# Performance work log

Hardware: AMD Instinct MI355X
Metric: run time of the kernel (lower is better)

Reference implementation:

```python
import jax, jax.numpy as jnp
import numpy as np

NC = 151  # number of object classes (VG)
NR = 51   # number of relation classes (VG)


def setup_inputs() -> dict:
    key = jax.random.key(0)
    ks = jax.random.split(key, 10)
    B, N, D = 32, 100, 4096
    H = D // 4
    w = lambda k, shape, fan_in: (jax.random.normal(k, shape, jnp.float32) / np.sqrt(fan_in).astype(np.float32))
    return {
        "encoder_reps": jax.random.normal(ks[0], (B * N, D), jnp.float32),
        "W_comp": w(ks[1], (D, H), D),        # obj_comp Linear (no bias)
        "W_ou1": w(ks[2], (H, H), H),         # ou1 Linear
        "W_ofc": w(ks[3], (H, H), H),         # ofc_u Linear
        "W_decomp": w(ks[4], (H, D), H),      # obj_decomp Linear
        "conv1": w(ks[5], (10, NR, 3, 3), NR * 9),  # Conv2d(51,10,3,pad=1)
        "conv2": w(ks[6], (5, 10, 3, 3), 10 * 9),   # Conv2d(10,5,3,pad=1)
        "conv3": w(ks[7], (1, 5, 1, 1), 5),         # Conv2d(5,1,1)
        "freq_emb": jax.random.normal(ks[8], (NC * NC, NR), jnp.float32) * 0.01,
        "obj_preds": jax.random.randint(ks[9], (B * N,), 0, NC),
        "num_obj": 100,
    }


def reference(encoder_reps, W_comp, W_ou1, W_ofc, W_decomp, conv1, conv2, conv3, freq_emb, obj_preds, num_obj):
    T, D = encoder_reps.shape
    N = num_obj
    B = T // N
    relu = jax.nn.relu
    # obj_comp then per-image ou1 (vectorized over images)
    comp = relu(encoder_reps @ W_comp).reshape(B, N, -1)   # [B,N,H]
    obj_u1 = relu(comp @ W_ou1)                             # [B,N,H]
    # product-index frequency-bias gather: emb[subj*NC + obj]
    labels = obj_preds.reshape(B, N)
    pair_idx = labels[:, :, None] * NC + labels[:, None, :]  # [B,N,N]
    adj_fg = freq_emb[pair_idx]                               # [B,N,N,NR]
    # adjacency net: Conv-Conv-Conv-Tanh over the NxN 'image' with NR channels
    x = jnp.transpose(adj_fg, (0, 3, 1, 2))                   # [B,NR,N,N]
    dn = ("NCHW", "OIHW", "NCHW")
    x = jax.lax.conv_general_dilated(x, conv1, (1, 1), "SAME", dimension_numbers=dn)
    x = jax.lax.conv_general_dilated(x, conv2, (1, 1), "SAME", dimension_numbers=dn)
    x = jnp.tanh(jax.lax.conv_general_dilated(x, conv3, (1, 1), "SAME", dimension_numbers=dn))
    adj = x[:, 0]                                             # [B,N,N]
    # graph message passing: adj @ obj_u1, then ofc_u / decomp + residual
    ofl_u = jnp.einsum("bnm,bmh->bnh", adj, obj_u1).reshape(T, -1)
    u_m = relu(ofl_u @ W_ofc)
    decomp = relu(u_m @ W_decomp)
    return decomp + encoder_reps
```

## Files before the change

### kernel.cpp

```cpp
#include <hip/hip_runtime.h>
#include <cmath>

#define NCC 151
#define NRCH 51
#define BDIM 32
#define NOBJ 100
#define DDIM 4096
#define HDIM 1024
#define TDIM (BDIM * NOBJ)

typedef __bf16 bf16_t;
typedef __bf16 bf16x8 __attribute__((ext_vector_type(8)));
typedef __bf16 bf16x4 __attribute__((ext_vector_type(4)));
typedef float f32x4 __attribute__((ext_vector_type(4)));

template <bool RELU, bool ADDBF16, int SPLITK, int MODE>
__global__ __launch_bounds__(256) void gemm_bf16(
    const bf16_t* __restrict__ A,
    const bf16_t* __restrict__ Bt,
    const bf16_t* __restrict__ add,
    void* __restrict__ Cout,
    int N, int K, size_t MN) {
  __shared__ __align__(16) bf16_t Asm[128 * 64];
  __shared__ __align__(16) bf16_t Bsm[128 * 64];
  const int tid = threadIdx.x;
  const int lane = tid & 63;
  const int w = tid >> 6;
  const int wm = w >> 1, wn = w & 1;

  const int nx = gridDim.x, ny = gridDim.y, nz = gridDim.z;
  const int h = blockIdx.x + nx * (blockIdx.y + ny * blockIdx.z);
  int bx, by, bz;
  if (MODE == 3) {
    const int xcd = h & 7, s = h >> 3;
    bz = xcd >> 1;
    const int half = xcd & 1;
    if (half == 1 && s >= 96) return;
    const int c = s / 40;
    if (c < 2) {
      const int within = s % 40;
      bx = within / 5;
      by = (half ? 13 : 0) + c * 5 + within % 5;
    } else if (half == 0) {
      const int w2 = s - 80;
      bx = w2 / 3;
      by = 10 + w2 % 3;
    } else {
      const int w2 = s - 80;
      bx = w2 / 2;
      by = 23 + w2 % 2;
    }
  } else {
    const int nwg = nx * ny * nz;
    const int q = nwg >> 3;
    const int lin = (h & 7) * q + (h >> 3);
    by = lin % ny;
    const int r = lin / ny;
    bx = r % nx;
    bz = r / nx;
  }

  const int bm = by * 128, bn = bx * 128;
  const int lr = lane & 15, lk = lane >> 4;

  int kBeg = 0, kEnd = K;
  if (SPLITK > 1) {
    const int chunk = (((K / 64) + SPLITK - 1) / SPLITK) * 64;
    kBeg = bz * chunk;
    kEnd = min(K, kBeg + chunk);
  }

  f32x4 acc[4][4];
#pragma unroll
  for (int m = 0; m < 4; ++m)
#pragma unroll
    for (int n = 0; n < 4; ++n) acc[m][n] = (f32x4){0.f, 0.f, 0.f, 0.f};

  const int srow = tid >> 3, sslot = tid & 7;
  char* ldsA = (char*)Asm;
  char* ldsB = (char*)Bsm;

  for (int kt = kBeg; kt < kEnd; kt += 64) {
    __syncthreads();
#pragma unroll
    for (int i = 0; i < 4; ++i) {
      const int row = i * 32 + srow;
      const int kc = sslot ^ (row & 7);
      const bf16_t* ga = A + (size_t)(bm + row) * K + kt + kc * 8;
      const bf16_t* gb = Bt + (size_t)(bn + row) * K + kt + kc * 8;
      __builtin_amdgcn_global_load_lds(
          (const __attribute__((address_space(1))) void*)ga,
          (__attribute__((address_space(3))) void*)(ldsA + i * 4096 + w * 1024),
          16, 0, 0);
      __builtin_amdgcn_global_load_lds(
          (const __attribute__((address_space(1))) void*)gb,
          (__attribute__((address_space(3))) void*)(ldsB + i * 4096 + w * 1024),
          16, 0, 0);
    }
    __syncthreads();

    bf16x8 af[4][2], bfr[4][2];
#pragma unroll
    for (int m = 0; m < 4; ++m) {
      const int row = wm * 64 + m * 16 + lr;
#pragma unroll
      for (int kk = 0; kk < 2; ++kk) {
        const int slot = kk * 4 + lk;
        af[m][kk] =
            *(const bf16x8*)(ldsA + row * 128 + ((slot ^ (lr & 7)) << 4));
      }
    }
#pragma unroll
    for (int n = 0; n < 4; ++n) {
      const int row = wn * 64 + n * 16 + lr;
#pragma unroll
      for (int kk = 0; kk < 2; ++kk) {
        const int slot = kk * 4 + lk;
        bfr[n][kk] =
            *(const bf16x8*)(ldsB + row * 128 + ((slot ^ (lr & 7)) << 4));
      }
    }
#pragma unroll
    for (int m = 0; m < 4; ++m)
#pragma unroll
      for (int n = 0; n < 4; ++n) {
        acc[m][n] = __builtin_amdgcn_mfma_f32_16x16x32_bf16(
            af[m][0], bfr[n][0], acc[m][n], 0, 0, 0);
        acc[m][n] = __builtin_amdgcn_mfma_f32_16x16x32_bf16(
            af[m][1], bfr[n][1], acc[m][n], 0, 0, 0);
      }
  }

  const int or0 = bm + wm * 64 + lk * 4;
  const int oc0 = bn + wn * 64 + lr;
#pragma unroll
  for (int m = 0; m < 4; ++m)
#pragma unroll
    for (int n = 0; n < 4; ++n)
#pragma unroll
      for (int r = 0; r < 4; ++r) {
        float v = acc[m][n][r];
        const size_t off = (size_t)(or0 + m * 16 + r) * N + (oc0 + n * 16);
        if (SPLITK > 1) {
          ((bf16_t*)Cout)[bz * MN + off] = (bf16_t)v;
        } else {
          if (RELU) v = fmaxf(v, 0.f);
          if (ADDBF16)
            ((float*)Cout)[off] = v + (float)add[off];
          else
            ((bf16_t*)Cout)[off] = (bf16_t)v;
        }
      }
}

template <int NPART>
__global__ __launch_bounds__(256) void reduceN_kernel(
    const bf16_t* __restrict__ p, bf16_t* __restrict__ out, int n8,
    size_t MN) {
  int i = blockIdx.x * 256 + threadIdx.x;
  if (i >= n8) return;
  float s[8] = {};
#pragma unroll
  for (int z = 0; z < NPART; ++z) {
    bf16x8 v = *(const bf16x8*)(p + z * MN + (size_t)i * 8);
#pragma unroll
    for (int j = 0; j < 8; ++j) s[j] += (float)v[j];
  }
  bf16x8 o;
#pragma unroll
  for (int j = 0; j < 8; ++j) o[j] = (bf16_t)fmaxf(s[j], 0.f);
  *(bf16x8*)(out + (size_t)i * 8) = o;
}

__global__ __launch_bounds__(256) void prep_all(
    const float* __restrict__ enc, const float* __restrict__ Wcomp,
    const float* __restrict__ Wou1, const float* __restrict__ Wofc,
    const float* __restrict__ Wdec, const float* __restrict__ w1,
    bf16_t* __restrict__ encb, bf16_t* __restrict__ WcompT,
    bf16_t* __restrict__ Wou1T, bf16_t* __restrict__ WofcT,
    bf16_t* __restrict__ WdecT, float* __restrict__ w1r) {
  __shared__ float t[32][33];
  const int tid = threadIdx.x;
  int blk = blockIdx.x;

  if (blk < 12800) {
    const int i = blk * 256 + tid;
    float4 v = ((const float4*)enc)[i];
    bf16x4 o = {(bf16_t)v.x, (bf16_t)v.y, (bf16_t)v.z, (bf16_t)v.w};
    ((bf16x4*)encb)[i] = o;
    return;
  }
  blk -= 12800;

  const float* in;
  bf16_t* out;
  int K, N, nx;
  if (blk < 4096) {
    in = Wcomp; out = WcompT; K = 4096; N = 1024; nx = 32;
  } else if (blk < 4096 + 1024) {
    blk -= 4096;
    in = Wou1; out = Wou1T; K = 1024; N = 1024; nx = 32;
  } else if (blk < 4096 + 2048) {
    blk -= 4096 + 1024;
    in = Wofc; out = WofcT; K = 1024; N = 1024; nx = 32;
  } else if (blk < 4096 + 2048 + 4096) {
    blk -= 4096 + 2048;
    in = Wdec; out = WdecT; K = 1024; N = 4096; nx = 128;
  } else {
    blk -= 4096 + 2048 + 4096;
    const int idx = blk * 256 + tid;
    if (idx < NRCH * 90) {
      int ci = idx / 90, r = idx % 90, k9 = r / 10, co = r % 10;
      w1r[idx] = w1[((co * NRCH + ci) * 3 + k9 / 3) * 3 + (k9 % 3)];
    }
    return;
  }

  const int n0 = (blk % nx) * 32, k0 = (blk / nx) * 32;
  const int tx = tid & 31, ty = tid >> 5;
#pragma unroll
  for (int i = 0; i < 4; ++i)
    t[ty + i * 8][tx] = in[(size_t)(k0 + ty + i * 8) * N + n0 + tx];
  __syncthreads();
#pragma unroll
  for (int i = 0; i < 4; ++i)
    out[(size_t)(n0 + ty + i * 8) * K + k0 + tx] = (bf16_t)t[tx][ty + i * 8];
}

__global__ __launch_bounds__(128) void femb1_kernel(
    const float* __restrict__ femb, const float* __restrict__ w1r,
    float* __restrict__ femb1) {
  __shared__ float row[NRCH];
  const int p = blockIdx.x;
  if (threadIdx.x < NRCH)
    row[threadIdx.x] = femb[(size_t)p * NRCH + threadIdx.x];
  __syncthreads();
  const int t = threadIdx.x;
  if (t >= 90) return;
  float acc = 0.f;
#pragma unroll
  for (int ci = 0; ci < NRCH; ++ci) acc += row[ci] * w1r[ci * 90 + t];
  femb1[((size_t)p * 9 + t / 10) * 12 + (t % 10)] = acc;
}

__global__ __launch_bounds__(256) void conv_fused(
    const int* __restrict__ preds, const float* __restrict__ femb1,
    const float* __restrict__ w2, const float* __restrict__ w3,
    float* __restrict__ adj) {
  __shared__ float xt[18][18][12];
  __shared__ float w[90];
  const int tid = threadIdx.x;
  const int b = blockIdx.z;
  const int ti = blockIdx.y * 16, tj = blockIdx.x * 16;

  if (tid < 90) {
    const int k9 = tid / 10, c2 = tid % 10;
    float a = 0.f;
#pragma unroll
    for (int c3 = 0; c3 < 5; ++c3)
      a += w3[c3] * w2[(c3 * 10 + c2) * 9 + k9];
    w[tid] = a;
  }

  const int* pr = preds + b * NOBJ;

  for (int t = tid; t < 324; t += 256) {
    const int hi = t / 18, wj = t % 18;
    const int ii = ti - 1 + hi, jj = tj - 1 + wj;
    f32x4 a0 = {0.f, 0.f, 0.f, 0.f}, a1 = a0, a2 = a0;
    if (ii >= 0 && ii < NOBJ && jj >= 0 && jj < NOBJ) {
#pragma unroll
      for (int kh = 0; kh < 3; ++kh) {
        const int i2 = ii + kh - 1;
        if (i2 < 0 || i2 >= NOBJ) continue;
        const int li = pr[i2];
#pragma unroll
        for (int kw = 0; kw < 3; ++kw) {
          const int j2 = jj + kw - 1;
          if (j2 < 0 || j2 >= NOBJ) continue;
          const int p = li * NCC + pr[j2];
          const f32x4* f =
              (const f32x4*)(femb1 + ((size_t)p * 9 + kh * 3 + kw) * 12);
          a0 += f[0];
          a1 += f[1];
          a2 += f[2];
        }
      }
    }
    f32x4* o = (f32x4*)&xt[hi][wj][0];
    o[0] = a0;
    o[1] = a1;
    o[2] = a2;
  }
  __syncthreads();

  const int di = tid >> 4, dj = tid & 15;
  const int i = ti + di, j = tj + dj;
  if (i >= NOBJ || j >= NOBJ) return;
  float acc = 0.f;
#pragma unroll
  for (int kh = 0; kh < 3; ++kh)
#pragma unroll
    for (int kw = 0; kw < 3; ++kw) {
      const float* xr = &xt[di + kh][dj + kw][0];
      const float* wr = w + (kh * 3 + kw) * 10;
#pragma unroll
      for (int c = 0; c < 10; ++c) acc += wr[c] * xr[c];
    }
  adj[((size_t)b * NOBJ + i) * NOBJ + j] = tanhf(acc);
}

__global__ __launch_bounds__(256) void einsum_mfma_kernel(
    const float* __restrict__ adj, const bf16_t* __restrict__ u1,
    bf16_t* __restrict__ ofl) {
  __shared__ __align__(16) bf16_t As[128 * 128];
  __shared__ __align__(16) bf16_t Us[128 * 128];
  const int b = blockIdx.y;
  const int h0 = blockIdx.x * 128;
  const int tid = threadIdx.x, lane = tid & 63, w = tid >> 6;
  const int wm = w >> 1, wn = w & 1;
  const int lr = lane & 15, lk = lane >> 4;

  {
    f32x4 z = {0.f, 0.f, 0.f, 0.f};
#pragma unroll
    for (int i = 0; i < 8; ++i) ((f32x4*)As)[tid + i * 256] = z;
#pragma unroll
    for (int i = 0; i < 8; ++i) ((f32x4*)Us)[tid + i * 256] = z;
  }
  __syncthreads();

  const float* ab = adj + (size_t)b * 10000;
#pragma unroll
  for (int i = 0; i < 10; ++i) {
    int idx = tid + i * 256;
    if (idx < 2500) {
      int row = idx / 25, kc = idx % 25;
      f32x4 v = ((const f32x4*)ab)[idx];
      bf16x4 o = {(bf16_t)v[0], (bf16_t)v[1], (bf16_t)v[2], (bf16_t)v[3]};
      int slot = kc >> 1;
      *(bf16x4*)((char*)As + row * 256 + ((slot ^ (row & 7)) << 4) +
                 (kc & 1) * 8) = o;
    }
  }

  const bf16_t* ub = u1 + (size_t)b * 100 * HDIM + h0;
#pragma unroll
  for (int i = 0; i < 7; ++i) {
    int idx = tid + i * 256;
    if (idx < 1600) {
      int hc = idx / 100, m = idx % 100;
      bf16x8 v = *(const bf16x8*)(ub + (size_t)m * HDIM + hc * 8);
      int slot = m >> 3, mr = m & 7;
#pragma unroll
      for (int j = 0; j < 8; ++j) {
        int h = hc * 8 + j;
        *((bf16_t*)((char*)Us + h * 256 + ((slot ^ (h & 7)) << 4) + mr * 2)) =
            v[j];
      }
    }
  }
  __syncthreads();

  f32x4 acc[4][4];
#pragma unroll
  for (int m = 0; m < 4; ++m)
#pragma unroll
    for (int n = 0; n < 4; ++n) acc[m][n] = (f32x4){0.f, 0.f, 0.f, 0.f};

#pragma unroll
  for (int ks = 0; ks < 4; ++ks) {
    bf16x8 a[4], u[4];
#pragma unroll
    for (int m = 0; m < 4; ++m) {
      int row = wm * 64 + m * 16 + lr;
      int slot = ks * 4 + lk;
      a[m] = *(const bf16x8*)((char*)As + row * 256 + ((slot ^ (lr & 7)) << 4));
    }
#pragma unroll
    for (int n = 0; n < 4; ++n) {
      int row = wn * 64 + n * 16 + lr;
      int slot = ks * 4 + lk;
      u[n] = *(const bf16x8*)((char*)Us + row * 256 + ((slot ^ (lr & 7)) << 4));
    }
#pragma unroll
    for (int m = 0; m < 4; ++m)
#pragma unroll
      for (int n = 0; n < 4; ++n)
        acc[m][n] = __builtin_amdgcn_mfma_f32_16x16x32_bf16(a[m], u[n],
                                                            acc[m][n], 0, 0, 0);
  }

  const int or0 = wm * 64 + lk * 4;
  const int oc0 = h0 + wn * 64 + lr;
#pragma unroll
  for (int m = 0; m < 4; ++m)
#pragma unroll
    for (int n = 0; n < 4; ++n)
#pragma unroll
      for (int r = 0; r < 4; ++r) {
        int row = or0 + m * 16 + r;
        if (row < 100)
          ofl[((size_t)b * 100 + row) * HDIM + oc0 + n * 16] =
              (bf16_t)acc[m][n][r];
      }
}

extern "C" void kernel_launch(void* const* d_in, const int* in_sizes, int n_in,
                              void* d_out, int out_size, void* d_ws,
                              size_t ws_size, hipStream_t stream) {
  const float* enc = (const float*)d_in[0];
  const float* W_comp = (const float*)d_in[1];
  const float* W_ou1 = (const float*)d_in[2];
  const float* W_ofc = (const float*)d_in[3];
  const float* W_dec = (const float*)d_in[4];
  const float* conv1w = (const float*)d_in[5];
  const float* conv2w = (const float*)d_in[6];
  const float* conv3w = (const float*)d_in[7];
  const float* femb = (const float*)d_in[8];
  const int* preds = (const int*)d_in[9];
  float* out = (float*)d_out;
  char* wsb = (char*)d_ws;

  const size_t MN = (size_t)TDIM * HDIM;

  bf16_t* encb   = (bf16_t*)(wsb + 0);
  bf16_t* WcompT = (bf16_t*)(wsb + 26214400);
  bf16_t* Wou1T  = (bf16_t*)(wsb + 34603008);
  bf16_t* WofcT  = (bf16_t*)(wsb + 36700160);
  bf16_t* WdecT  = (bf16_t*)(wsb + 38797312);
  float*  w1r    = (float*)(wsb + 47185920);
  bf16_t* comp   = (bf16_t*)(wsb + 47204352);
  bf16_t* part4  = (bf16_t*)(wsb + 53757952);
  float*  femb1  = (float*)(wsb + 53757952);
  bf16_t* obj_u1 = (bf16_t*)(wsb + 63608064);
  float*  adj    = (float*)(wsb + 70161664);
  bf16_t* u_m    = (bf16_t*)(wsb + 71441664);
  bf16_t* ofl_u  = (bf16_t*)(wsb + 47204352);

  const int n8 = (int)(MN / 8);

  prep_all<<<23058, 256, 0, stream>>>(enc, W_comp, W_ou1, W_ofc, W_dec,
                                      conv1w, encb, WcompT, Wou1T, WofcT,
                                      WdecT, w1r);

  gemm_bf16<false, false, 4, 3><<<dim3(832, 1, 1), 256, 0, stream>>>(
      encb, WcompT, nullptr, part4, HDIM, DDIM, MN);
  reduceN_kernel<4><<<n8 / 256, 256, 0, stream>>>(part4, comp, n8, MN);

  gemm_bf16<true, false, 1, 0>
      <<<dim3(HDIM / 128, TDIM / 128), 256, 0, stream>>>(
          comp, Wou1T, nullptr, obj_u1, HDIM, HDIM, MN);

  femb1_kernel<<<NCC * NCC, 128, 0, stream>>>(femb, w1r, femb1);
  conv_fused<<<dim3(7, 7, BDIM), 256, 0, stream>>>(preds, femb1, conv2w,
                                                   conv3w, adj);

  einsum_mfma_kernel<<<dim3(HDIM / 128, BDIM), 256, 0, stream>>>(adj, obj_u1,
                                                                 ofl_u);

  gemm_bf16<true, false, 1, 0>
      <<<dim3(HDIM / 128, TDIM / 128), 256, 0, stream>>>(
          ofl_u, WofcT, nullptr, u_m, HDIM, HDIM, MN);

  gemm_bf16<true, true, 1, 0>
      <<<dim3(DDIM / 128, TDIM / 128), 256, 0, stream>>>(
          u_m, WdecT, encb, out, DDIM, HDIM, MN);
}
```

Baseline: 243.2 us.

## Co-schedule conv1 precompute with split-K GEMM and reduce with conv

```diff
diff --git a/kernel.cpp b/kernel.cpp
--- a/kernel.cpp
+++ b/kernel.cpp
@@ -8,6 +8,7 @@
 #define DDIM 4096
 #define HDIM 1024
 #define TDIM (BDIM * NOBJ)
+#define NPAIR (NCC * NCC)
 
 typedef __bf16 bf16_t;
 typedef __bf16 bf16x8 __attribute__((ext_vector_type(8)));
@@ -16,10 +17,8 @@
 
 template <bool RELU, bool ADDBF16, int SPLITK, int MODE>
 __global__ __launch_bounds__(256) void gemm_bf16(
-    const bf16_t* __restrict__ A,
-    const bf16_t* __restrict__ Bt,
-    const bf16_t* __restrict__ add,
-    void* __restrict__ Cout,
+    const bf16_t* __restrict__ A, const bf16_t* __restrict__ Bt,
+    const bf16_t* __restrict__ add, void* __restrict__ Cout,
     int N, int K, size_t MN) {
   __shared__ __align__(16) bf16_t Asm[128 * 64];
   __shared__ __align__(16) bf16_t Bsm[128 * 64];
@@ -31,26 +30,7 @@
   const int nx = gridDim.x, ny = gridDim.y, nz = gridDim.z;
   const int h = blockIdx.x + nx * (blockIdx.y + ny * blockIdx.z);
   int bx, by, bz;
-  if (MODE == 3) {
-    const int xcd = h & 7, s = h >> 3;
-    bz = xcd >> 1;
-    const int half = xcd & 1;
-    if (half == 1 && s >= 96) return;
-    const int c = s / 40;
-    if (c < 2) {
-      const int within = s % 40;
-      bx = within / 5;
-      by = (half ? 13 : 0) + c * 5 + within % 5;
-    } else if (half == 0) {
-      const int w2 = s - 80;
-      bx = w2 / 3;
-      by = 10 + w2 % 3;
-    } else {
-      const int w2 = s - 80;
-      bx = w2 / 2;
-      by = 23 + w2 % 2;
-    }
-  } else {
+  {
     const int nwg = nx * ny * nz;
     const int q = nwg >> 3;
     const int lin = (h & 7) * q + (h >> 3);
@@ -153,112 +133,180 @@
       }
 }
 
-template <int NPART>
-__global__ __launch_bounds__(256) void reduceN_kernel(
-    const bf16_t* __restrict__ p, bf16_t* __restrict__ out, int n8,
+__global__ __launch_bounds__(256) void fused_g1_femb1(
+    const bf16_t* __restrict__ A,
+    const bf16_t* __restrict__ Bt,
+    bf16_t* __restrict__ part4,
+    const float* __restrict__ femb,
+    const float* __restrict__ w1,
+    float* __restrict__ femb1,
     size_t MN) {
-  int i = blockIdx.x * 256 + threadIdx.x;
-  if (i >= n8) return;
-  float s[8] = {};
-#pragma unroll
-  for (int z = 0; z < NPART; ++z) {
-    bf16x8 v = *(const bf16x8*)(p + z * MN + (size_t)i * 8);
-#pragma unroll
-    for (int j = 0; j < 8; ++j) s[j] += (float)v[j];
-  }
-  bf16x8 o;
-#pragma unroll
-  for (int j = 0; j < 8; ++j) o[j] = (bf16_t)fmaxf(s[j], 0.f);
-  *(bf16x8*)(out + (size_t)i * 8) = o;
-}
-
-__global__ __launch_bounds__(256) void prep_all(
-    const float* __restrict__ enc, const float* __restrict__ Wcomp,
-    const float* __restrict__ Wou1, const float* __restrict__ Wofc,
-    const float* __restrict__ Wdec, const float* __restrict__ w1,
-    bf16_t* __restrict__ encb, bf16_t* __restrict__ WcompT,
-    bf16_t* __restrict__ Wou1T, bf16_t* __restrict__ WofcT,
-    bf16_t* __restrict__ WdecT, float* __restrict__ w1r) {
-  __shared__ float t[32][33];
   const int tid = threadIdx.x;
   int blk = blockIdx.x;
 
-  if (blk < 12800) {
-    const int i = blk * 256 + tid;
-    float4 v = ((const float4*)enc)[i];
-    bf16x4 o = {(bf16_t)v.x, (bf16_t)v.y, (bf16_t)v.z, (bf16_t)v.w};
-    ((bf16x4*)encb)[i] = o;
+  if (blk >= 832) {
+    __shared__ float w1s[10 * NRCH * 9];
+    __shared__ float rows[2][NRCH];
+    for (int t = tid; t < 10 * NRCH * 9; t += 256) w1s[t] = w1[t];
+    const int p0 = (blk - 832) * 2;
+    const int hi = tid >> 7;
+    const int t2 = tid & 127;
+    const int p = p0 + hi;
+    if (t2 < NRCH && p < NPAIR)
+      rows[hi][t2] = femb[(size_t)p * NRCH + t2];
+    __syncthreads();
+    if (t2 >= 90 || p >= NPAIR) return;
+    const int k9 = t2 / 10, co = t2 % 10;
+    float acc = 0.f;
+#pragma unroll
+    for (int ci = 0; ci < NRCH; ++ci)
+      acc += rows[hi][ci] * w1s[(co * NRCH + ci) * 9 + k9];
+    femb1[((size_t)p * 9 + k9) * 12 + co] = acc;
     return;
   }
-  blk -= 12800;
-
-  const float* in;
-  bf16_t* out;
-  int K, N, nx;
-  if (blk < 4096) {
-    in = Wcomp; out = WcompT; K = 4096; N = 1024; nx = 32;
-  } else if (blk < 4096 + 1024) {
-    blk -= 4096;
-    in = Wou1; out = Wou1T; K = 1024; N = 1024; nx = 32;
-  } else if (blk < 4096 + 2048) {
-    blk -= 4096 + 1024;
-    in = Wofc; out = WofcT; K = 1024; N = 1024; nx = 32;
-  } else if (blk < 4096 + 2048 + 4096) {
-    blk -= 4096 + 2048;
-    in = Wdec; out = WdecT; K = 1024; N = 4096; nx = 128;
+
+  __shared__ __align__(16) bf16_t Asm[128 * 64];
+  __shared__ __align__(16) bf16_t Bsm[128 * 64];
+  const int lane = tid & 63;
+  const int w = tid >> 6;
+  const int wm = w >> 1, wn = w & 1;
+
+  const int xcd = blk & 7, s = blk >> 3;
+  const int bz = xcd >> 1;
+  const int half = xcd & 1;
+  if (half == 1 && s >= 96) return;
+  int bx, by;
+  const int c = s / 40;
+  if (c < 2) {
+    const int within = s % 40;
+    bx = within / 5;
+    by = (half ? 13 : 0) + c * 5 + within % 5;
+  } else if (half == 0) {
+    const int w2 = s - 80;
+    bx = w2 / 3;
+    by = 10 + w2 % 3;
   } else {
-    blk -= 4096 + 2048 + 4096;
-    const int idx = blk * 256 + tid;
-    if (idx < NRCH * 90) {
-      int ci = idx / 90, r = idx % 90, k9 = r / 10, co = r % 10;
-      w1r[idx] = w1[((co * NRCH + ci) * 3 + k9 / 3) * 3 + (k9 % 3)];
-    }
-    return;
-  }
-
-  const int n0 = (blk % nx) * 32, k0 = (blk / nx) * 32;
-  const int tx = tid & 31, ty = tid >> 5;
-#pragma unroll
-  for (int i = 0; i < 4; ++i)
-    t[ty + i * 8][tx] = in[(size_t)(k0 + ty + i * 8) * N + n0 + tx];
-  __syncthreads();
-#pragma unroll
-  for (int i = 0; i < 4; ++i)
-    out[(size_t)(n0 + ty + i * 8) * K + k0 + tx] = (bf16_t)t[tx][ty + i * 8];
+    const int w2 = s - 80;
+    bx = w2 / 2;
+    by = 23 + w2 % 2;
+  }
+
+  const int K = DDIM, N = HDIM;
+  const int bm = by * 128, bn = bx * 128;
+  const int lr = lane & 15, lk = lane >> 4;
+  const int kBeg = bz * 1024, kEnd = kBeg + 1024;
+
+  f32x4 acc[4][4];
+#pragma unroll
+  for (int m = 0; m < 4; ++m)
+#pragma unroll
+    for (int n = 0; n < 4; ++n) acc[m][n] = (f32x4){0.f, 0.f, 0.f, 0.f};
+
+  const int srow = tid >> 3, sslot = tid & 7;
+  char* ldsA = (char*)Asm;
+  char* ldsB = (char*)Bsm;
+
+  for (int kt = kBeg; kt < kEnd; kt += 64) {
+    __syncthreads();
+#pragma unroll
+    for (int i = 0; i < 4; ++i) {
+      const int row = i * 32 + srow;
+      const int kc = sslot ^ (row & 7);
+      const bf16_t* ga = A + (size_t)(bm + row) * K + kt + kc * 8;
+      const bf16_t* gb = Bt + (size_t)(bn + row) * K + kt + kc * 8;
+      __builtin_amdgcn_global_load_lds(
+          (const __attribute__((address_space(1))) void*)ga,
+          (__attribute__((address_space(3))) void*)(ldsA + i * 4096 + w * 1024),
+          16, 0, 0);
+      __builtin_amdgcn_global_load_lds(
+          (const __attribute__((address_space(1))) void*)gb,
+          (__attribute__((address_space(3))) void*)(ldsB + i * 4096 + w * 1024),
+          16, 0, 0);
+    }
+    __syncthreads();
+
+    bf16x8 af[4][2], bfr[4][2];
+#pragma unroll
+    for (int m = 0; m < 4; ++m) {
+      const int row = wm * 64 + m * 16 + lr;
+#pragma unroll
+      for (int kk = 0; kk < 2; ++kk) {
+        const int slot = kk * 4 + lk;
+        af[m][kk] =
+            *(const bf16x8*)(ldsA + row * 128 + ((slot ^ (lr & 7)) << 4));
+      }
+    }
+#pragma unroll
+    for (int n = 0; n < 4; ++n) {
+      const int row = wn * 64 + n * 16 + lr;
+#pragma unroll
+      for (int kk = 0; kk < 2; ++kk) {
+        const int slot = kk * 4 + lk;
+        bfr[n][kk] =
+            *(const bf16x8*)(ldsB + row * 128 + ((slot ^ (lr & 7)) << 4));
+      }
+    }
+#pragma unroll
+    for (int m = 0; m < 4; ++m)
+#pragma unroll
+      for (int n = 0; n < 4; ++n) {
+        acc[m][n] = __builtin_amdgcn_mfma_f32_16x16x32_bf16(
+            af[m][0], bfr[n][0], acc[m][n], 0, 0, 0);
+        acc[m][n] = __builtin_amdgcn_mfma_f32_16x16x32_bf16(
+            af[m][1], bfr[n][1], acc[m][n], 0, 0, 0);
+      }
+  }
+
+  const int or0 = bm + wm * 64 + lk * 4;
+  const int oc0 = bn + wn * 64 + lr;
+#pragma unroll
+  for (int m = 0; m < 4; ++m)
+#pragma unroll
+    for (int n = 0; n < 4; ++n)
+#pragma unroll
+      for (int r = 0; r < 4; ++r) {
+        const size_t off = (size_t)(or0 + m * 16 + r) * N + (oc0 + n * 16);
+        part4[bz * MN + off] = (bf16_t)acc[m][n][r];
+      }
 }
 
-__global__ __launch_bounds__(128) void femb1_kernel(
-    const float* __restrict__ femb, const float* __restrict__ w1r,
-    float* __restrict__ femb1) {
-  __shared__ float row[NRCH];
-  const int p = blockIdx.x;
-  if (threadIdx.x < NRCH)
-    row[threadIdx.x] = femb[(size_t)p * NRCH + threadIdx.x];
-  __syncthreads();
-  const int t = threadIdx.x;
-  if (t >= 90) return;
-  float acc = 0.f;
-#pragma unroll
-  for (int ci = 0; ci < NRCH; ++ci) acc += row[ci] * w1r[ci * 90 + t];
-  femb1[((size_t)p * 9 + t / 10) * 12 + (t % 10)] = acc;
-}
-
-__global__ __launch_bounds__(256) void conv_fused(
+__global__ __launch_bounds__(256) void fused_red_conv(
+    const bf16_t* __restrict__ part4, bf16_t* __restrict__ comp, size_t MN,
     const int* __restrict__ preds, const float* __restrict__ femb1,
     const float* __restrict__ w2, const float* __restrict__ w3,
     float* __restrict__ adj) {
+  const int tid = threadIdx.x;
+  int blk = blockIdx.x;
+
+  if (blk < 1600) {
+    const int i = blk * 256 + tid;
+    float s[8] = {};
+#pragma unroll
+    for (int z = 0; z < 4; ++z) {
+      bf16x8 v = *(const bf16x8*)(part4 + z * MN + (size_t)i * 8);
+#pragma unroll
+      for (int j = 0; j < 8; ++j) s[j] += (float)v[j];
+    }
+    bf16x8 o;
+#pragma unroll
+    for (int j = 0; j < 8; ++j) o[j] = (bf16_t)fmaxf(s[j], 0.f);
+    *(bf16x8*)(comp + (size_t)i * 8) = o;
+    return;
+  }
+
+  blk -= 1600;
+  const int b = blk / 49;
+  const int rem = blk % 49;
+  const int ti = (rem / 7) * 16, tj = (rem % 7) * 16;
+
   __shared__ float xt[18][18][12];
   __shared__ float w[90];
-  const int tid = threadIdx.x;
-  const int b = blockIdx.z;
-  const int ti = blockIdx.y * 16, tj = blockIdx.x * 16;
 
   if (tid < 90) {
     const int k9 = tid / 10, c2 = tid % 10;
     float a = 0.f;
 #pragma unroll
-    for (int c3 = 0; c3 < 5; ++c3)
-      a += w3[c3] * w2[(c3 * 10 + c2) * 9 + k9];
+    for (int c3 = 0; c3 < 5; ++c3) a += w3[c3] * w2[(c3 * 10 + c2) * 9 + k9];
     w[tid] = a;
   }
 
@@ -308,6 +356,52 @@
       for (int c = 0; c < 10; ++c) acc += wr[c] * xr[c];
     }
   adj[((size_t)b * NOBJ + i) * NOBJ + j] = tanhf(acc);
+}
+
+__global__ __launch_bounds__(256) void prep_all(
+    const float* __restrict__ enc, const float* __restrict__ Wcomp,
+    const float* __restrict__ Wou1, const float* __restrict__ Wofc,
+    const float* __restrict__ Wdec, bf16_t* __restrict__ encb,
+    bf16_t* __restrict__ WcompT, bf16_t* __restrict__ Wou1T,
+    bf16_t* __restrict__ WofcT, bf16_t* __restrict__ WdecT) {
+  __shared__ float t[32][33];
+  const int tid = threadIdx.x;
+  int blk = blockIdx.x;
+
+  if (blk < 12800) {
+    const int i = blk * 256 + tid;
+    float4 v = ((const float4*)enc)[i];
+    bf16x4 o = {(bf16_t)v.x, (bf16_t)v.y, (bf16_t)v.z, (bf16_t)v.w};
+    ((bf16x4*)encb)[i] = o;
+    return;
+  }
+  blk -= 12800;
+
+  const float* in;
+  bf16_t* out;
+  int K, N, nx;
+  if (blk < 4096) {
+    in = Wcomp; out = WcompT; K = 4096; N = 1024; nx = 32;
+  } else if (blk < 5120) {
+    blk -= 4096;
+    in = Wou1; out = Wou1T; K = 1024; N = 1024; nx = 32;
+  } else if (blk < 6144) {
+    blk -= 5120;
+    in = Wofc; out = WofcT; K = 1024; N = 1024; nx = 32;
+  } else {
+    blk -= 6144;
+    in = Wdec; out = WdecT; K = 1024; N = 4096; nx = 128;
+  }
+
+  const int n0 = (blk % nx) * 32, k0 = (blk / nx) * 32;
+  const int tx = tid & 31, ty = tid >> 5;
+#pragma unroll
+  for (int i = 0; i < 4; ++i)
+    t[ty + i * 8][tx] = in[(size_t)(k0 + ty + i * 8) * N + n0 + tx];
+  __syncthreads();
+#pragma unroll
+  for (int i = 0; i < 4; ++i)
+    out[(size_t)(n0 + ty + i * 8) * K + k0 + tx] = (bf16_t)t[tx][ty + i * 8];
 }
 
 __global__ __launch_bounds__(256) void einsum_mfma_kernel(
@@ -429,32 +523,26 @@
   bf16_t* Wou1T  = (bf16_t*)(wsb + 34603008);
   bf16_t* WofcT  = (bf16_t*)(wsb + 36700160);
   bf16_t* WdecT  = (bf16_t*)(wsb + 38797312);
-  float*  w1r    = (float*)(wsb + 47185920);
-  bf16_t* comp   = (bf16_t*)(wsb + 47204352);
-  bf16_t* part4  = (bf16_t*)(wsb + 53757952);
-  float*  femb1  = (float*)(wsb + 53757952);
-  bf16_t* obj_u1 = (bf16_t*)(wsb + 63608064);
-  float*  adj    = (float*)(wsb + 70161664);
-  bf16_t* u_m    = (bf16_t*)(wsb + 71441664);
-  bf16_t* ofl_u  = (bf16_t*)(wsb + 47204352);
-
-  const int n8 = (int)(MN / 8);
-
-  prep_all<<<23058, 256, 0, stream>>>(enc, W_comp, W_ou1, W_ofc, W_dec,
-                                      conv1w, encb, WcompT, Wou1T, WofcT,
-                                      WdecT, w1r);
-
-  gemm_bf16<false, false, 4, 3><<<dim3(832, 1, 1), 256, 0, stream>>>(
-      encb, WcompT, nullptr, part4, HDIM, DDIM, MN);
-  reduceN_kernel<4><<<n8 / 256, 256, 0, stream>>>(part4, comp, n8, MN);
+  bf16_t* comp   = (bf16_t*)(wsb + 47185920);
+  bf16_t* part4  = (bf16_t*)(wsb + 53739520);
+  float*  femb1  = (float*)(wsb + 79953920);
+  bf16_t* obj_u1 = (bf16_t*)(wsb + 53739520);
+  float*  adj    = (float*)(wsb + 60293120);
+  bf16_t* u_m    = (bf16_t*)(wsb + 61573120);
+  bf16_t* ofl_u  = (bf16_t*)(wsb + 47185920);
+
+  prep_all<<<23040, 256, 0, stream>>>(enc, W_comp, W_ou1, W_ofc, W_dec, encb,
+                                      WcompT, Wou1T, WofcT, WdecT);
+
+  fused_g1_femb1<<<832 + 11401, 256, 0, stream>>>(encb, WcompT, part4, femb,
+                                                  conv1w, femb1, MN);
+
+  fused_red_conv<<<1600 + 1568, 256, 0, stream>>>(
+      part4, comp, MN, preds, femb1, conv2w, conv3w, adj);
 
   gemm_bf16<true, false, 1, 0>
       <<<dim3(HDIM / 128, TDIM / 128), 256, 0, stream>>>(
           comp, Wou1T, nullptr, obj_u1, HDIM, HDIM, MN);
-
-  femb1_kernel<<<NCC * NCC, 128, 0, stream>>>(femb, w1r, femb1);
-  conv_fused<<<dim3(7, 7, BDIM), 256, 0, stream>>>(preds, femb1, conv2w,
-                                                   conv3w, adj);
 
   einsum_mfma_kernel<<<dim3(HDIM / 128, BDIM), 256, 0, stream>>>(adj, obj_u1,
                                                                  ofl_u);
```

After: 263.7 us. +8.4%, slower.
